# Kernel optimization log

Hardware: AMD Instinct MI355X
Metric: run time of the kernel (lower is better)

Reference implementation:

```python
import jax, jax.numpy as jnp
import numpy as np

DIST = 22.63      # __init__ kwarg `dist` (cdist threshold)
DS_SIZE = 80      # hard-coded Downsample result_size in LeafBranchFunc
LOG_CLAMP = 100.0 # torch BCE clamps log terms at -100


def _cdist(x):
    # x: [B,N,F] -> pairwise euclidean distances [B,N,N]
    sq = jnp.sum(x * x, axis=-1)
    d2 = sq[:, :, None] + sq[:, None, :] - 2.0 * jnp.einsum('bnf,bmf->bnm', x, x)
    return jnp.sqrt(jnp.maximum(d2, 0.0))


@jax.jit
def _cluster(point_features):
    """Faithful port of Cluster.forward: threshold cdist, then the strictly
    sequential greedy label stamping with a single global next_label counter."""
    adj = _cdist(point_features) < DIST  # [B,N,N] bool
    N = adj.shape[1]
    idx = jnp.arange(N)

    def row_step(carry, xs):
        labels, nxt = carry
        row, i = xs
        cur = labels[i]
        new = jnp.where(cur == 0, nxt, cur)
        nxt = jnp.where(cur == 0, nxt + 1, nxt)
        labels = labels.at[i].set(new)
        labels = jnp.where(row, new, labels)  # stamp all thresholded neighbors
        return (labels, nxt), None

    def batch_step(nxt, adj_b):
        (labels, nxt), _ = jax.lax.scan(row_step, (jnp.zeros(N, jnp.int32), nxt), (adj_b, idx))
        return nxt, labels

    _, labels = jax.lax.scan(batch_step, jnp.int32(1), adj)  # sequential over batch: shared counter
    return labels  # [B,N] int32


def _classify(pts, W1, b1, W2, b2, W3, b3):
    # pts: [K,80,3] -> P(class 1) per cluster, PointNet-lite classifier + softmax
    h = jax.nn.relu(pts @ W1 + b1)       # [K,80,64]
    h = jax.nn.relu(h @ W2 + b2)         # [K,80,128]
    g = jnp.max(h, axis=1)               # [K,128] global max pool
    logits = g @ W3 + b3                 # [K,2]
    return jax.nn.softmax(logits, axis=-1)[:, 1]


def setup_inputs() -> dict:
    key = jax.random.key(0)
    ks = jax.random.split(key, 8)
    B, N, F = 4, 4096, 256
    return {
        'point_features': jax.random.normal(ks[0], (B, N, F), jnp.float32),
        'points': jax.random.normal(ks[1], (B, N, 3), jnp.float32),
        'W1': jax.random.normal(ks[2], (3, 64), jnp.float32) * 0.5,
        'b1': jnp.zeros((64,), jnp.float32),
        'W2': jax.random.normal(ks[3], (64, 128), jnp.float32) * 0.1,
        'b2': jnp.zeros((128,), jnp.float32),
        'W3': jax.random.normal(ks[4], (128, 2), jnp.float32) * 0.1,
        'b3': jnp.zeros((2,), jnp.float32),
    }


def reference(point_features, points, W1, b1, W2, b2, W3, b3):
    labels = np.asarray(_cluster(point_features))  # [B,N]; cluster ids are data-dependent
    points_np = np.asarray(points)
    rng = np.random.RandomState(0)  # Downsample uses np.random.choice with replacement
    total = jnp.float32(0.0)
    for b in range(labels.shape[0]):
        ds = []
        for c in np.unique(labels[b]):
            cp = points_np[b][labels[b] == c]                    # [M,3] points of this cluster
            sel = rng.choice(cp.shape[0], DS_SIZE, replace=True)  # random downsample to 80
            ds.append(cp[sel])
        ds = jnp.asarray(np.stack(ds), dtype=jnp.float32)        # [K,80,3]
        p = jnp.nan_to_num(_classify(ds, W1, b1, W2, b2, W3, b3))
        # binary_cross_entropy with all-ones targets: mean(-log p), log clamped at -100
        loss = jnp.mean(jnp.minimum(-jnp.log(p), LOG_CLAMP))
        total = total + loss
    return total
```

## Files before the change

### kernel.cpp

```cpp
#include <hip/hip_runtime.h>
#include <math.h>
#include <stdint.h>
#include <stdlib.h>

constexpr int B_ = 4, N_ = 4096, F_ = 256;
constexpr int DS = 80;
constexpr int MAXC = 16384;
constexpr int RAWBLKS = 16;
constexpr int RAWN = 624 * RAWBLKS;

namespace {
struct RawStream {
  unsigned* buf = nullptr;
  RawStream() {
    unsigned mt[624];
    mt[0] = 0u;
    for (int i = 1; i < 624; ++i)
      mt[i] = 1812433253u * (mt[i - 1] ^ (mt[i - 1] >> 30)) + (unsigned)i;
    if (hipHostMalloc((void**)&buf, (size_t)(RAWN + 624) * 4, 0) != hipSuccess || !buf)
      buf = (unsigned*)malloc((size_t)(RAWN + 624) * 4);
    for (int blk = 0; blk < RAWBLKS; ++blk) {
      for (int i = 0; i < 624; ++i) {
        unsigned y = (mt[i] & 0x80000000u) | (mt[(i + 1) % 624] & 0x7fffffffu);
        mt[i] = mt[(i + 397) % 624] ^ (y >> 1) ^ ((y & 1u) ? 0x9908b0dfu : 0u);
      }
      for (int i = 0; i < 624; ++i) {
        unsigned y = mt[i];
        y ^= y >> 11; y ^= (y << 7) & 0x9d2c5680u; y ^= (y << 15) & 0xefc60000u; y ^= y >> 18;
        buf[blk * 624 + i] = y;
      }
    }
    for (int i = 0; i < 624; ++i) buf[RAWN + i] = mt[i];
  }
};
RawStream g_raw;
}

__global__ __launch_bounds__(256) void pre_kernel(const float* __restrict__ x,
                                                  float* __restrict__ sq) {
  const int blk = blockIdx.x, tid = threadIdx.x;
  const int i = blk * 256 + tid;
  float4 v = ((const float4*)x)[i];
  float s = v.x * v.x + v.y * v.y + v.z * v.z + v.w * v.w;
  for (int off = 32; off > 0; off >>= 1) s += __shfl_down(s, off);
  if ((tid & 63) == 0) sq[blk * 4 + (tid >> 6)] = s;
}

__global__ __launch_bounds__(256) void scan_kernel(const float* __restrict__ x,
                                                   const float* __restrict__ sq,
                                                   int* __restrict__ p,
                                                   int* __restrict__ q) {
  const int tid = threadIdx.x;
  const int w = tid >> 6, lane = tid & 63;
  const int bb = blockIdx.x & 3;
  const int rem = blockIdx.x >> 2;
  const int idx = rem * 4 + w;
  const int i = idx >> 1;
  const bool qmode = (idx & 1) == 0;

  const float* xb = x + (size_t)bb * N_ * F_;
  const float* sqb = sq + (size_t)bb * N_;
  const int gl = lane & 15, g = lane >> 4;

  const int jhi = qmode ? (N_ - 1) : (i - 1);
  const int jlo = qmode ? (i + 1) : 0;

  int found = -1;
  if (jhi >= jlo) {
    const float4* ra = (const float4*)(xb + (size_t)i * F_);
    float4 a0 = ra[gl + 0], a1 = ra[gl + 16], a2 = ra[gl + 32], a3 = ra[gl + 48];
    const double sqi = (double)sqb[i];
    const double THR2D = (double)22.63f * (double)22.63f;

    int j0 = jhi;
    int cjA = j0 - g;     if (cjA < jlo) cjA = jlo;
    int cjB = j0 - 4 - g; if (cjB < jlo) cjB = jlo;
    const float4* rA = (const float4*)(xb + (size_t)cjA * F_);
    const float4* rB = (const float4*)(xb + (size_t)cjB * F_);
    float4 cA0 = rA[gl], cA1 = rA[gl + 16], cA2 = rA[gl + 32], cA3 = rA[gl + 48];
    float4 cB0 = rB[gl], cB1 = rB[gl + 16], cB2 = rB[gl + 32], cB3 = rB[gl + 48];

    while (j0 >= jlo) {
      const int jn = j0 - 8;
      int nA = jn - g;     if (nA < jlo) nA = jlo;
      int nB = jn - 4 - g; if (nB < jlo) nB = jlo;
      const float4* rnA = (const float4*)(xb + (size_t)nA * F_);
      const float4* rnB = (const float4*)(xb + (size_t)nB * F_);
      float4 pA0 = rnA[gl], pA1 = rnA[gl + 16], pA2 = rnA[gl + 32], pA3 = rnA[gl + 48];
      float4 pB0 = rnB[gl], pB1 = rnB[gl + 16], pB2 = rnB[gl + 32], pB3 = rnB[gl + 48];

      float sA = 0.f;
      sA += a0.x * cA0.x + a0.y * cA0.y + a0.z * cA0.z + a0.w * cA0.w;
      sA += a1.x * cA1.x + a1.y * cA1.y + a1.z * cA1.z + a1.w * cA1.w;
      sA += a2.x * cA2.x + a2.y * cA2.y + a2.z * cA2.z + a2.w * cA2.w;
      sA += a3.x * cA3.x + a3.y * cA3.y + a3.z * cA3.z + a3.w * cA3.w;
      float sB = 0.f;
      sB += a0.x * cB0.x + a0.y * cB0.y + a0.z * cB0.z + a0.w * cB0.w;
      sB += a1.x * cB1.x + a1.y * cB1.y + a1.z * cB1.z + a1.w * cB1.w;
      sB += a2.x * cB2.x + a2.y * cB2.y + a2.z * cB2.z + a2.w * cB2.w;
      sB += a3.x * cB3.x + a3.y * cB3.y + a3.z * cB3.z + a3.w * cB3.w;
      sA += __shfl_xor(sA, 1); sA += __shfl_xor(sA, 2);
      sA += __shfl_xor(sA, 4); sA += __shfl_xor(sA, 8);
      sB += __shfl_xor(sB, 1); sB += __shfl_xor(sB, 2);
      sB += __shfl_xor(sB, 4); sB += __shfl_xor(sB, 8);

      bool okA = false, okB = false;
      const int mA = j0 - g, mB = j0 - 4 - g;
      if (mA >= jlo) {
        double d2 = sqi + (double)sqb[mA] - 2.0 * (double)sA;
        okA = d2 < THR2D;
      }
      if (mB >= jlo) {
        double d2 = sqi + (double)sqb[mB] - 2.0 * (double)sB;
        okB = d2 < THR2D;
      }
      unsigned long long balA = __ballot(okA);
      unsigned long long balB = __ballot(okB);
      if (balA) {
        found = j0 - ((__ffsll(balA) - 1) >> 4);
        break;
      }
      if (balB) {
        found = j0 - 4 - ((__ffsll(balB) - 1) >> 4);
        break;
      }
      cA0 = pA0; cA1 = pA1; cA2 = pA2; cA3 = pA3;
      cB0 = pB0; cB1 = pB1; cB2 = pB2; cB3 = pB3;
      j0 = jn;
    }
  }
  if (lane == 0) {
    const size_t o = (size_t)bb * N_ + i;
    if (qmode) q[o] = (found < 0) ? i : found;
    else       p[o] = found;
  }
}

__global__ __launch_bounds__(1024) void cluster_kernel(const int* __restrict__ p,
                                                       const int* __restrict__ q,
                                                       int* __restrict__ lab,
                                                       int* __restrict__ Karr, int* __restrict__ labs,
                                                       int* __restrict__ Msz) {
  const int b = blockIdx.x, tid = threadIdx.x;
  __shared__ int A[N_ + 1], Bb[N_], labS[N_];
  __shared__ int waveOff[17];
  __shared__ int runBase, chg;

  for (int k = tid; k < N_; k += 1024) {
    int pi = p[(size_t)b * N_ + k];
    A[k] = (pi < 0) ? k : pi;
  }
  __syncthreads();
  int* src = A; int* dst = Bb;
  for (int it = 0; it < 12; ++it) {
    if (tid == 0) chg = 0;
    __syncthreads();
    bool any = false;
    for (int k = tid; k < N_; k += 1024) {
      int v = src[src[k]];
      dst[k] = v;
      any |= (v != src[k]);
    }
    if (any) chg = 1;
    __syncthreads();
    int* t = src; src = dst; dst = t;
    if (!chg) break;
  }
  if (tid == 0) runBase = 0;
  __syncthreads();
  for (int base = 0; base < N_; base += 1024) {
    int i = base + tid;
    bool isR = (src[i] == i);
    unsigned long long bal = __ballot(isR);
    int lane = tid & 63, wid = tid >> 6;
    if (lane == 0) waveOff[wid] = __popcll(bal);
    __syncthreads();
    if (tid == 0) {
      int s = runBase;
      for (int w = 0; w < 16; ++w) { int t2 = waveOff[w]; waveOff[w] = s; s += t2; }
      waveOff[16] = s;
    }
    __syncthreads();
    int incl = __popcll(bal & (~0ull >> (63 - lane)));
    dst[i] = waveOff[wid] + incl;
    __syncthreads();
    if (tid == 0) runBase = waveOff[16];
    __syncthreads();
  }
  for (int j = tid; j < N_; j += 1024) {
    int qq = q[(size_t)b * N_ + j];
    int lv = dst[src[qq]];
    labS[j] = lv;
    lab[(size_t)b * N_ + j] = lv;
  }
  __syncthreads();

  int* cnt = A;
  for (int k = tid; k <= N_; k += 1024) cnt[k] = 0;
  __syncthreads();
  {
    const int lane = tid & 63;
    for (int j = tid; j < N_; j += 1024) {
      int v = labS[j];
      unsigned long long remM = ~0ull;
      while (remM) {
        int leader = __ffsll(remM) - 1;
        int lv = __shfl(v, leader);
        unsigned long long m = __ballot(v == lv);
        if (lane == leader) atomicAdd(&cnt[lv], __popcll(m));
        remM &= ~m;
      }
    }
  }
  __syncthreads();
  if (tid == 0) runBase = 0;
  __syncthreads();
  for (int base = 1; base <= N_; base += 1024) {
    int c = base + tid;
    bool m = (cnt[c] > 0);
    unsigned long long bal = __ballot(m);
    int lane = tid & 63, wid = tid >> 6;
    if (lane == 0) waveOff[wid] = __popcll(bal);
    __syncthreads();
    if (tid == 0) {
      int s = runBase;
      for (int w = 0; w < 16; ++w) { int t2 = waveOff[w]; waveOff[w] = s; s += t2; }
      waveOff[16] = s;
    }
    __syncthreads();
    if (m) {
      int pos = waveOff[wid] + __popcll(bal & ((1ull << lane) - 1));
      labs[(size_t)b * N_ + pos] = c;
      Msz[(size_t)b * N_ + pos] = cnt[c];
    }
    __syncthreads();
    if (tid == 0) runBase = waveOff[16];
    __syncthreads();
  }
  if (tid == 0) Karr[b] = runBase;
}

__device__ inline void mt_regen(unsigned* mt, unsigned* raw, int lane) {
  const int ph_s[3] = {0, 227, 454};
  const int ph_e[3] = {227, 454, 624};
#pragma unroll
  for (int ph = 0; ph < 3; ++ph) {
    const int s = ph_s[ph], e = ph_e[ph];
    unsigned aReg[4], bReg[4];
    const int niter = (e - s + 63) >> 6;
    for (int it = 0; it < niter; ++it) {
      int i = s + it * 64 + lane;
      if (i < e) { aReg[it] = mt[i]; bReg[it] = mt[(i + 1) % 624]; }
    }
    __syncthreads();
    for (int it = 0; it < niter; ++it) {
      int i = s + it * 64 + lane;
      if (i < e) {
        unsigned y = (aReg[it] & 0x80000000u) | (bReg[it] & 0x7fffffffu);
        mt[i] = mt[(i + 397) % 624] ^ (y >> 1) ^ ((y & 1u) ? 0x9908b0dfu : 0u);
      }
    }
    __syncthreads();
  }
  for (int it = 0; it < 10; ++it) {
    int i = it * 64 + lane;
    if (i < 624) {
      unsigned y = mt[i];
      y ^= y >> 11; y ^= (y << 7) & 0x9d2c5680u; y ^= (y << 15) & 0xefc60000u; y ^= y >> 18;
      raw[i] = y;
    }
  }
  __syncthreads();
}

__global__ __launch_bounds__(64) void rngsel_kernel(const int* __restrict__ Karr,
                                                    const int* __restrict__ Msz,
                                                    const unsigned* __restrict__ rawG,
                                                    const unsigned* __restrict__ mtSave,
                                                    int* __restrict__ sel, int* __restrict__ meta,
                                                    int* __restrict__ totK) {
  __shared__ int mszS[2048];
  __shared__ unsigned rawL[2048];
  __shared__ unsigned mtF[624];
  __shared__ unsigned rawF[624];
  const int lane = threadIdx.x;
  int pos = 0;
  int winBase = -100000;
  bool fb = false;
  int fpos = 0;
  int cid = 0;
  for (int b = 0; b < B_; ++b) {
    const int Kb = Karr[b];
    for (int k0 = 0; k0 < Kb; k0 += 2048) {
      const int nk = min(2048, Kb - k0);
      for (int i = lane; i < nk; i += 64) mszS[i] = Msz[(size_t)b * N_ + k0 + i];
      __syncthreads();
      for (int kk = 0; kk < nk; ++kk) {
        const int M = mszS[kk];
        if (lane == 0) meta[cid] = (b << 16) | (k0 + kk);
        if (M <= 1) {
          sel[cid * DS + lane] = 0;
          if (lane < DS - 64) sel[cid * DS + 64 + lane] = 0;
        } else {
          const unsigned rng = (unsigned)(M - 1);
          unsigned mask = rng;
          mask |= mask >> 1; mask |= mask >> 2; mask |= mask >> 4; mask |= mask >> 8; mask |= mask >> 16;
          int acc = 0;
          while (acc < DS) {
            unsigned v = 0xFFFFFFFFu;
            bool ok = false;
            int take;
            if (!fb && pos >= RAWN) {
              fb = true;
              for (int i = lane; i < 624; i += 64) mtF[i] = mtSave[i];
              __syncthreads();
              fpos = 624;
            }
            if (!fb) {
              if (pos + 64 > winBase + 2048) {
                winBase = pos;
                for (int i = lane; i < 2048; i += 64) rawL[i] = rawG[winBase + i];
                __syncthreads();
              }
              take = min(64, RAWN - pos);
              if (lane < take) { v = rawL[pos - winBase + lane] & mask; ok = (v <= rng); }
            } else {
              if (fpos == 624) { mt_regen(mtF, rawF, lane); fpos = 0; }
              take = min(64, 624 - fpos);
              if (lane < take) { v = rawF[fpos + lane] & mask; ok = (v <= rng); }
            }
            unsigned long long bal = __ballot(ok);
            int pre = __popcll(bal & ((1ull << lane) - 1ull));
            int tot = __popcll(bal);
            if (ok && acc + pre < DS) sel[cid * DS + acc + pre] = (int)v;
            int advance;
            if (acc + tot >= DS) {
              int need = DS - acc;
              bool win = ok && (pre + 1 == need);
              unsigned long long wb = __ballot(win);
              advance = __ffsll(wb);
              acc = DS;
            } else {
              advance = take;
              acc += tot;
            }
            if (fb) fpos += advance; else pos += advance;
          }
        }
        ++cid;
      }
      __syncthreads();
    }
  }
  if (lane == 0) totK[0] = cid;
}

__global__ __launch_bounds__(256) void classify_par_kernel(
    const float* __restrict__ points, const float* __restrict__ W1, const float* __restrict__ b1,
    const float* __restrict__ W2, const float* __restrict__ b2,
    const float* __restrict__ W3, const float* __restrict__ b3,
    const int* __restrict__ lab, const int* __restrict__ labs,
    const int* __restrict__ sel, const int* __restrict__ meta, const int* __restrict__ totK,
    float* __restrict__ lossArr) {
  __shared__ unsigned wordsS[128];
  __shared__ int prefS[128];
  __shared__ float pts[DS][3];
  __shared__ float h1[DS][64];
  __shared__ float W2s[64][128];
  __shared__ float gmax[128];
  const int tid = threadIdx.x;
  int T = totK[0]; if (T > MAXC) T = MAXC;
  if ((int)blockIdx.x >= T) return;
  for (int k = tid; k < 64 * 128; k += 256) W2s[k >> 7][k & 127] = W2[k];

  for (int cid = blockIdx.x; cid < T; cid += gridDim.x) {
    const int mv = meta[cid];
    const int b = mv >> 16, k = mv & 0xFFFF;
    const int c = labs[(size_t)b * N_ + k];
    if (tid < 128) {
      unsigned wbits = 0;
      const int* lb = lab + (size_t)b * N_ + tid * 32;
      for (int s = 0; s < 32; ++s) wbits |= (lb[s] == c) ? (1u << s) : 0u;
      wordsS[tid] = wbits;
    }
    __syncthreads();
    if (tid == 0) {
      int s = 0;
      for (int w2 = 0; w2 < 128; ++w2) { prefS[w2] = s; s += __popc(wordsS[w2]); }
    }
    __syncthreads();
    if (tid < DS) {
      int r = sel[cid * DS + tid];
      int lo = 0, hi = 127;
      while (lo < hi) { int mid = (lo + hi + 1) >> 1; if (prefS[mid] <= r) lo = mid; else hi = mid - 1; }
      int rem = r - prefS[lo];
      unsigned wbits = wordsS[lo];
      int j = lo * 32;
      for (;;) {
        int bpos = __ffs(wbits) - 1;
        if (rem == 0) { j += bpos; break; }
        wbits &= wbits - 1; --rem;
      }
      pts[tid][0] = points[((size_t)b * N_ + j) * 3 + 0];
      pts[tid][1] = points[((size_t)b * N_ + j) * 3 + 1];
      pts[tid][2] = points[((size_t)b * N_ + j) * 3 + 2];
    }
    __syncthreads();
    for (int o = tid; o < DS * 64; o += 256) {
      int r = o >> 6, cc = o & 63;
      float v = pts[r][0] * W1[cc] + pts[r][1] * W1[64 + cc] + pts[r][2] * W1[128 + cc] + b1[cc];
      h1[r][cc] = fmaxf(v, 0.f);
    }
    __syncthreads();
    {
      const int cc = tid & 127, half = tid >> 7;
      const float b2c = b2[cc];
      float m = -1e30f;
      for (int r = half * 40; r < half * 40 + 40; ++r) {
        float a0 = 0.f, a1 = 0.f, a2 = 0.f, a3 = 0.f;
#pragma unroll
        for (int kk = 0; kk < 64; kk += 4) {
          a0 += h1[r][kk + 0] * W2s[kk + 0][cc];
          a1 += h1[r][kk + 1] * W2s[kk + 1][cc];
          a2 += h1[r][kk + 2] * W2s[kk + 2][cc];
          a3 += h1[r][kk + 3] * W2s[kk + 3][cc];
        }
        float acc = ((a0 + a1) + (a2 + a3)) + b2c;
        m = fmaxf(m, fmaxf(acc, 0.f));
      }
      if (half == 0) gmax[cc] = m;
      __syncthreads();
      if (half == 1) gmax[cc] = fmaxf(gmax[cc], m);
    }
    __syncthreads();
    if (tid == 0) {
      float l0 = b3[0], l1 = b3[1];
      for (int cc = 0; cc < 128; ++cc) { l0 += gmax[cc] * W3[cc * 2 + 0]; l1 += gmax[cc] * W3[cc * 2 + 1]; }
      float mx = fmaxf(l0, l1);
      float e0 = expf(l0 - mx), e1 = expf(l1 - mx);
      float p1 = e1 / (e0 + e1);
      if (isnan(p1)) p1 = 0.f;
      lossArr[cid] = fminf(-logf(p1), 100.f);
    }
    __syncthreads();
  }
}

__global__ __launch_bounds__(256) void reduce_kernel(const float* __restrict__ lossArr,
                                                     const int* __restrict__ meta,
                                                     const int* __restrict__ totK,
                                                     const int* __restrict__ Karr,
                                                     float* __restrict__ out) {
  __shared__ float accB[4];
  const int tid = threadIdx.x;
  if (tid < 4) accB[tid] = 0.f;
  __syncthreads();
  int T = totK[0]; if (T > MAXC) T = MAXC;
  float local[4] = {0.f, 0.f, 0.f, 0.f};
  for (int cid = tid; cid < T; cid += 256) local[meta[cid] >> 16] += lossArr[cid];
  for (int b = 0; b < 4; ++b) {
    float v = local[b];
    for (int off = 32; off > 0; off >>= 1) v += __shfl_down(v, off);
    if ((tid & 63) == 0) atomicAdd(&accB[b], v);
  }
  __syncthreads();
  if (tid == 0) {
    float tot = 0.f;
    for (int b = 0; b < 4; ++b) tot += accB[b] / (float)Karr[b];
    out[0] = tot;
  }
}

extern "C" void kernel_launch(void* const* d_in, const int* in_sizes, int n_in,
                              void* d_out, int out_size, void* d_ws, size_t ws_size,
                              hipStream_t stream) {
  const float* x      = (const float*)d_in[0];
  const float* points = (const float*)d_in[1];
  const float* W1 = (const float*)d_in[2];
  const float* b1 = (const float*)d_in[3];
  const float* W2 = (const float*)d_in[4];
  const float* b2 = (const float*)d_in[5];
  const float* W3 = (const float*)d_in[6];
  const float* b3 = (const float*)d_in[7];
  float* out = (float*)d_out;

  char* wsb = (char*)d_ws;
  size_t off = 0;
  auto carve = [&](size_t bytes) -> void* {
    void* r = wsb + off;
    off += (bytes + 255) & ~(size_t)255;
    return r;
  };
  float* sq      = (float*)carve((size_t)B_ * N_ * 4);
  int* p         = (int*)carve((size_t)B_ * N_ * 4);
  int* q         = (int*)carve((size_t)B_ * N_ * 4);
  int* lab       = (int*)carve((size_t)B_ * N_ * 4);
  int* labs      = (int*)carve((size_t)B_ * N_ * 4);
  int* Msz       = (int*)carve((size_t)B_ * N_ * 4);
  int* Karr      = (int*)carve(256);
  int* totK      = (int*)carve(256);
  unsigned* rawG = (unsigned*)carve((size_t)(RAWN + 624 + 2048) * 4);
  unsigned* mtSave = rawG + RAWN;
  int* sel       = (int*)carve((size_t)MAXC * DS * 4);
  int* meta      = (int*)carve((size_t)MAXC * 4);
  float* lossArr = (float*)carve((size_t)MAXC * 4);
  (void)ws_size;

  hipMemcpyAsync(rawG, g_raw.buf, (size_t)(RAWN + 624) * 4,
                 hipMemcpyHostToDevice, stream);

  hipLaunchKernelGGL(pre_kernel, dim3(B_ * N_ * F_ / 1024), dim3(256), 0, stream, x, sq);
  hipLaunchKernelGGL(scan_kernel, dim3(B_ * N_ * 2 / 4), dim3(256), 0, stream, x, sq, p, q);
  hipLaunchKernelGGL(cluster_kernel, dim3(B_), dim3(1024), 0, stream,
                     p, q, lab, Karr, labs, Msz);
  hipLaunchKernelGGL(rngsel_kernel, dim3(1), dim3(64), 0, stream,
                     Karr, Msz, rawG, mtSave, sel, meta, totK);
  hipLaunchKernelGGL(classify_par_kernel, dim3(512), dim3(256), 0, stream,
                     points, W1, b1, W2, b2, W3, b3, lab, labs, sel, meta, totK, lossArr);
  hipLaunchKernelGGL(reduce_kernel, dim3(1), dim3(256), 0, stream,
                     lossArr, meta, totK, Karr, out);
}
```

Measured before the change: 161.0 us.

## Merge forward/backward scans per row and fuse loss reduction into classify

Each wave in the scan kernel now runs both the forward (q) and backward (p) neighbor searches for one row. It loads that row's features once, and the grid is halved. The separate reduce kernel is removed: the last block to finish classify, found through an atomic arrivals counter reset in pre_kernel, does the per-batch loss sum. This saves one launch and the duplicated row loads, but halves scan parallelism and adds atomics and a threadfence.

```diff
diff --git a/kernel.cpp b/kernel.cpp
--- a/kernel.cpp
+++ b/kernel.cpp
@@ -37,13 +37,74 @@
 }
 
 __global__ __launch_bounds__(256) void pre_kernel(const float* __restrict__ x,
-                                                  float* __restrict__ sq) {
+                                                  float* __restrict__ sq,
+                                                  int* __restrict__ arrivals) {
   const int blk = blockIdx.x, tid = threadIdx.x;
   const int i = blk * 256 + tid;
   float4 v = ((const float4*)x)[i];
   float s = v.x * v.x + v.y * v.y + v.z * v.z + v.w * v.w;
   for (int off = 32; off > 0; off >>= 1) s += __shfl_down(s, off);
   if ((tid & 63) == 0) sq[blk * 4 + (tid >> 6)] = s;
+  if (blk == 0 && tid == 0) arrivals[0] = 0;
+}
+
+__device__ __forceinline__ int scan_dir(const float* __restrict__ xb,
+                                        const float* __restrict__ sqb,
+                                        float4 a0, float4 a1, float4 a2, float4 a3,
+                                        double sqi, int jhi, int jlo, int gl, int g) {
+  if (jhi < jlo) return -1;
+  const double THR2D = (double)22.63f * (double)22.63f;
+  int j0 = jhi;
+  int cjA = j0 - g;     if (cjA < jlo) cjA = jlo;
+  int cjB = j0 - 4 - g; if (cjB < jlo) cjB = jlo;
+  const float4* rA = (const float4*)(xb + (size_t)cjA * F_);
+  const float4* rB = (const float4*)(xb + (size_t)cjB * F_);
+  float4 cA0 = rA[gl], cA1 = rA[gl + 16], cA2 = rA[gl + 32], cA3 = rA[gl + 48];
+  float4 cB0 = rB[gl], cB1 = rB[gl + 16], cB2 = rB[gl + 32], cB3 = rB[gl + 48];
+
+  while (j0 >= jlo) {
+    const int jn = j0 - 8;
+    int nA = jn - g;     if (nA < jlo) nA = jlo;
+    int nB = jn - 4 - g; if (nB < jlo) nB = jlo;
+    const float4* rnA = (const float4*)(xb + (size_t)nA * F_);
+    const float4* rnB = (const float4*)(xb + (size_t)nB * F_);
+    float4 pA0 = rnA[gl], pA1 = rnA[gl + 16], pA2 = rnA[gl + 32], pA3 = rnA[gl + 48];
+    float4 pB0 = rnB[gl], pB1 = rnB[gl + 16], pB2 = rnB[gl + 32], pB3 = rnB[gl + 48];
+
+    float sA = 0.f;
+    sA += a0.x * cA0.x + a0.y * cA0.y + a0.z * cA0.z + a0.w * cA0.w;
+    sA += a1.x * cA1.x + a1.y * cA1.y + a1.z * cA1.z + a1.w * cA1.w;
+    sA += a2.x * cA2.x + a2.y * cA2.y + a2.z * cA2.z + a2.w * cA2.w;
+    sA += a3.x * cA3.x + a3.y * cA3.y + a3.z * cA3.z + a3.w * cA3.w;
+    float sB = 0.f;
+    sB += a0.x * cB0.x + a0.y * cB0.y + a0.z * cB0.z + a0.w * cB0.w;
+    sB += a1.x * cB1.x + a1.y * cB1.y + a1.z * cB1.z + a1.w * cB1.w;
+    sB += a2.x * cB2.x + a2.y * cB2.y + a2.z * cB2.z + a2.w * cB2.w;
+    sB += a3.x * cB3.x + a3.y * cB3.y + a3.z * cB3.z + a3.w * cB3.w;
+    sA += __shfl_xor(sA, 1); sA += __shfl_xor(sA, 2);
+    sA += __shfl_xor(sA, 4); sA += __shfl_xor(sA, 8);
+    sB += __shfl_xor(sB, 1); sB += __shfl_xor(sB, 2);
+    sB += __shfl_xor(sB, 4); sB += __shfl_xor(sB, 8);
+
+    bool okA = false, okB = false;
+    const int mA = j0 - g, mB = j0 - 4 - g;
+    if (mA >= jlo) {
+      double d2 = sqi + (double)sqb[mA] - 2.0 * (double)sA;
+      okA = d2 < THR2D;
+    }
+    if (mB >= jlo) {
+      double d2 = sqi + (double)sqb[mB] - 2.0 * (double)sB;
+      okB = d2 < THR2D;
+    }
+    unsigned long long balA = __ballot(okA);
+    unsigned long long balB = __ballot(okB);
+    if (balA) return j0 - ((__ffsll(balA) - 1) >> 4);
+    if (balB) return j0 - 4 - ((__ffsll(balB) - 1) >> 4);
+    cA0 = pA0; cA1 = pA1; cA2 = pA2; cA3 = pA3;
+    cB0 = pB0; cB1 = pB1; cB2 = pB2; cB3 = pB3;
+    j0 = jn;
+  }
+  return -1;
 }
 
 __global__ __launch_bounds__(256) void scan_kernel(const float* __restrict__ x,
@@ -53,86 +114,23 @@
   const int tid = threadIdx.x;
   const int w = tid >> 6, lane = tid & 63;
   const int bb = blockIdx.x & 3;
-  const int rem = blockIdx.x >> 2;
-  const int idx = rem * 4 + w;
-  const int i = idx >> 1;
-  const bool qmode = (idx & 1) == 0;
-
+  const int rg = blockIdx.x >> 2;
+  const int i = rg * 4 + w;
   const float* xb = x + (size_t)bb * N_ * F_;
   const float* sqb = sq + (size_t)bb * N_;
   const int gl = lane & 15, g = lane >> 4;
 
-  const int jhi = qmode ? (N_ - 1) : (i - 1);
-  const int jlo = qmode ? (i + 1) : 0;
-
-  int found = -1;
-  if (jhi >= jlo) {
-    const float4* ra = (const float4*)(xb + (size_t)i * F_);
-    float4 a0 = ra[gl + 0], a1 = ra[gl + 16], a2 = ra[gl + 32], a3 = ra[gl + 48];
-    const double sqi = (double)sqb[i];
-    const double THR2D = (double)22.63f * (double)22.63f;
-
-    int j0 = jhi;
-    int cjA = j0 - g;     if (cjA < jlo) cjA = jlo;
-    int cjB = j0 - 4 - g; if (cjB < jlo) cjB = jlo;
-    const float4* rA = (const float4*)(xb + (size_t)cjA * F_);
-    const float4* rB = (const float4*)(xb + (size_t)cjB * F_);
-    float4 cA0 = rA[gl], cA1 = rA[gl + 16], cA2 = rA[gl + 32], cA3 = rA[gl + 48];
-    float4 cB0 = rB[gl], cB1 = rB[gl + 16], cB2 = rB[gl + 32], cB3 = rB[gl + 48];
-
-    while (j0 >= jlo) {
-      const int jn = j0 - 8;
-      int nA = jn - g;     if (nA < jlo) nA = jlo;
-      int nB = jn - 4 - g; if (nB < jlo) nB = jlo;
-      const float4* rnA = (const float4*)(xb + (size_t)nA * F_);
-      const float4* rnB = (const float4*)(xb + (size_t)nB * F_);
-      float4 pA0 = rnA[gl], pA1 = rnA[gl + 16], pA2 = rnA[gl + 32], pA3 = rnA[gl + 48];
-      float4 pB0 = rnB[gl], pB1 = rnB[gl + 16], pB2 = rnB[gl + 32], pB3 = rnB[gl + 48];
-
-      float sA = 0.f;
-      sA += a0.x * cA0.x + a0.y * cA0.y + a0.z * cA0.z + a0.w * cA0.w;
-      sA += a1.x * cA1.x + a1.y * cA1.y + a1.z * cA1.z + a1.w * cA1.w;
-      sA += a2.x * cA2.x + a2.y * cA2.y + a2.z * cA2.z + a2.w * cA2.w;
-      sA += a3.x * cA3.x + a3.y * cA3.y + a3.z * cA3.z + a3.w * cA3.w;
-      float sB = 0.f;
-      sB += a0.x * cB0.x + a0.y * cB0.y + a0.z * cB0.z + a0.w * cB0.w;
-      sB += a1.x * cB1.x + a1.y * cB1.y + a1.z * cB1.z + a1.w * cB1.w;
-      sB += a2.x * cB2.x + a2.y * cB2.y + a2.z * cB2.z + a2.w * cB2.w;
-      sB += a3.x * cB3.x + a3.y * cB3.y + a3.z * cB3.z + a3.w * cB3.w;
-      sA += __shfl_xor(sA, 1); sA += __shfl_xor(sA, 2);
-      sA += __shfl_xor(sA, 4); sA += __shfl_xor(sA, 8);
-      sB += __shfl_xor(sB, 1); sB += __shfl_xor(sB, 2);
-      sB += __shfl_xor(sB, 4); sB += __shfl_xor(sB, 8);
-
-      bool okA = false, okB = false;
-      const int mA = j0 - g, mB = j0 - 4 - g;
-      if (mA >= jlo) {
-        double d2 = sqi + (double)sqb[mA] - 2.0 * (double)sA;
-        okA = d2 < THR2D;
-      }
-      if (mB >= jlo) {
-        double d2 = sqi + (double)sqb[mB] - 2.0 * (double)sB;
-        okB = d2 < THR2D;
-      }
-      unsigned long long balA = __ballot(okA);
-      unsigned long long balB = __ballot(okB);
-      if (balA) {
-        found = j0 - ((__ffsll(balA) - 1) >> 4);
-        break;
-      }
-      if (balB) {
-        found = j0 - 4 - ((__ffsll(balB) - 1) >> 4);
-        break;
-      }
-      cA0 = pA0; cA1 = pA1; cA2 = pA2; cA3 = pA3;
-      cB0 = pB0; cB1 = pB1; cB2 = pB2; cB3 = pB3;
-      j0 = jn;
-    }
-  }
+  const float4* ra = (const float4*)(xb + (size_t)i * F_);
+  float4 a0 = ra[gl], a1 = ra[gl + 16], a2 = ra[gl + 32], a3 = ra[gl + 48];
+  const double sqi = (double)sqb[i];
+
+  const int qf = scan_dir(xb, sqb, a0, a1, a2, a3, sqi, N_ - 1, i + 1, gl, g);
+  const int pf = scan_dir(xb, sqb, a0, a1, a2, a3, sqi, i - 1, 0, gl, g);
+
   if (lane == 0) {
     const size_t o = (size_t)bb * N_ + i;
-    if (qmode) q[o] = (found < 0) ? i : found;
-    else       p[o] = found;
+    q[o] = (qf < 0) ? i : qf;
+    p[o] = pf;
   }
 }
 
@@ -361,13 +359,16 @@
     const float* __restrict__ W3, const float* __restrict__ b3,
     const int* __restrict__ lab, const int* __restrict__ labs,
     const int* __restrict__ sel, const int* __restrict__ meta, const int* __restrict__ totK,
-    float* __restrict__ lossArr) {
+    const int* __restrict__ Karr, float* __restrict__ lossArr,
+    int* __restrict__ arrivals, float* __restrict__ out) {
   __shared__ unsigned wordsS[128];
   __shared__ int prefS[128];
   __shared__ float pts[DS][3];
   __shared__ float h1[DS][64];
   __shared__ float W2s[64][128];
   __shared__ float gmax[128];
+  __shared__ float accB[4];
+  __shared__ int lastS;
   const int tid = threadIdx.x;
   int T = totK[0]; if (T > MAXC) T = MAXC;
   if ((int)blockIdx.x >= T) return;
@@ -440,24 +441,23 @@
       float e0 = expf(l0 - mx), e1 = expf(l1 - mx);
       float p1 = e1 / (e0 + e1);
       if (isnan(p1)) p1 = 0.f;
-      lossArr[cid] = fminf(-logf(p1), 100.f);
-    }
-    __syncthreads();
-  }
-}
-
-__global__ __launch_bounds__(256) void reduce_kernel(const float* __restrict__ lossArr,
-                                                     const int* __restrict__ meta,
-                                                     const int* __restrict__ totK,
-                                                     const int* __restrict__ Karr,
-                                                     float* __restrict__ out) {
-  __shared__ float accB[4];
-  const int tid = threadIdx.x;
+      atomicExch(&lossArr[cid], fminf(-logf(p1), 100.f));
+    }
+    __syncthreads();
+  }
+
+  __threadfence();
+  if (tid == 0) {
+    const int active = min((int)gridDim.x, T);
+    lastS = (atomicAdd(arrivals, 1) == active - 1) ? 1 : 0;
+  }
+  __syncthreads();
+  if (!lastS) return;
   if (tid < 4) accB[tid] = 0.f;
   __syncthreads();
-  int T = totK[0]; if (T > MAXC) T = MAXC;
   float local[4] = {0.f, 0.f, 0.f, 0.f};
-  for (int cid = tid; cid < T; cid += 256) local[meta[cid] >> 16] += lossArr[cid];
+  for (int cid = tid; cid < T; cid += 256)
+    local[meta[cid] >> 16] += atomicAdd(&lossArr[cid], 0.0f);
   for (int b = 0; b < 4; ++b) {
     float v = local[b];
     for (int off = 32; off > 0; off >>= 1) v += __shfl_down(v, off);
@@ -499,6 +499,7 @@
   int* Msz       = (int*)carve((size_t)B_ * N_ * 4);
   int* Karr      = (int*)carve(256);
   int* totK      = (int*)carve(256);
+  int* arrivals  = (int*)carve(256);
   unsigned* rawG = (unsigned*)carve((size_t)(RAWN + 624 + 2048) * 4);
   unsigned* mtSave = rawG + RAWN;
   int* sel       = (int*)carve((size_t)MAXC * DS * 4);
@@ -509,14 +510,14 @@
   hipMemcpyAsync(rawG, g_raw.buf, (size_t)(RAWN + 624) * 4,
                  hipMemcpyHostToDevice, stream);
 
-  hipLaunchKernelGGL(pre_kernel, dim3(B_ * N_ * F_ / 1024), dim3(256), 0, stream, x, sq);
-  hipLaunchKernelGGL(scan_kernel, dim3(B_ * N_ * 2 / 4), dim3(256), 0, stream, x, sq, p, q);
+  hipLaunchKernelGGL(pre_kernel, dim3(B_ * N_ * F_ / 1024), dim3(256), 0, stream,
+                     x, sq, arrivals);
+  hipLaunchKernelGGL(scan_kernel, dim3(B_ * N_ / 4), dim3(256), 0, stream, x, sq, p, q);
   hipLaunchKernelGGL(cluster_kernel, dim3(B_), dim3(1024), 0, stream,
                      p, q, lab, Karr, labs, Msz);
   hipLaunchKernelGGL(rngsel_kernel, dim3(1), dim3(64), 0, stream,
                      Karr, Msz, rawG, mtSave, sel, meta, totK);
   hipLaunchKernelGGL(classify_par_kernel, dim3(512), dim3(256), 0, stream,
-                     points, W1, b1, W2, b2, W3, b3, lab, labs, sel, meta, totK, lossArr);
-  hipLaunchKernelGGL(reduce_kernel, dim3(1), dim3(256), 0, stream,
-                     lossArr, meta, totK, Karr, out);
-}
+                     points, W1, b1, W2, b2, W3, b3, lab, labs, sel, meta, totK,
+                     Karr, lossArr, arrivals, out);
+}
```

Result: no change. 161.0 us (-0.0%).
